# Kernel tuning notes

Measured on AMD Instinct MI355X. Metric: run time of the kernel, lower is better.

Reference implementation:

```python
import jax, jax.numpy as jnp
import numpy as np

DIM = 1024


def setup_inputs() -> dict:
    key = jax.random.key(0)
    ks = jax.random.split(key, 9)
    s = 1.0 / np.sqrt(DIM)
    x = jax.random.normal(ks[0], (4, 4096, DIM), dtype=jnp.float32)
    Wq = jax.random.uniform(ks[1], (DIM, DIM), jnp.float32, -s, s)
    bq = jax.random.uniform(ks[2], (DIM,), jnp.float32, -s, s)
    Wk = jax.random.uniform(ks[3], (DIM, DIM), jnp.float32, -s, s)
    bk = jax.random.uniform(ks[4], (DIM,), jnp.float32, -s, s)
    Wv = jax.random.uniform(ks[5], (DIM, DIM), jnp.float32, -s, s)
    bv = jax.random.uniform(ks[6], (DIM,), jnp.float32, -s, s)
    Wo = jax.random.uniform(ks[7], (DIM, DIM), jnp.float32, -s, s)
    bo = jax.random.uniform(ks[8], (DIM,), jnp.float32, -s, s)
    return {"x": x, "Wq": Wq, "bq": bq, "Wk": Wk, "bk": bk,
            "Wv": Wv, "bv": bv, "Wo": Wo, "bo": bo}


def reference(x, Wq, bq, Wk, bk, Wv, bv, Wo, bo):
    # x: [B, N, C]; weights stored as [C, C] (torch Linear applies x @ W.T,
    # here we store W already transposed so x @ W matches).
    scale = x.shape[-1] ** (-0.5)
    q = x @ Wq + bq                                  # [B, N, C]
    k = x @ Wk + bk
    v = x @ Wv + bv
    scores = jnp.einsum('bnc,bmc->bnm', q, k) * scale  # [B, N, N]
    attn = jax.nn.softmax(scores, axis=-1)
    out = jnp.einsum('bnm,bmc->bnc', attn, v)          # [B, N, C]
    return out @ Wo + bo
```

## Files before the change

kernel.cpp:

```cpp
#include <hip/hip_runtime.h>
#include <hip/hip_bf16.h>
#include <stdint.h>

typedef __bf16 bf16_8 __attribute__((ext_vector_type(8)));
typedef float  f32x4  __attribute__((ext_vector_type(4)));

#define GLL(g, l) __builtin_amdgcn_global_load_lds(                         \
    (__attribute__((address_space(1))) void*)(g),                           \
    (__attribute__((address_space(3))) void*)(l), 16, 0, 0)

__global__ void sniff_dtype(const uint32_t* __restrict__ x, uint32_t* __restrict__ flag)
{
    uint32_t w = x[threadIdx.x];
    uint32_t e = (w >> 23) & 0xFF;
    int isf32 = (e >= 100 && e <= 145) ? 1 : 0;
    unsigned long long m = __ballot(isf32);
    if (threadIdx.x == 0) *flag = (__popcll(m) >= 48) ? 1u : 0u;
}

__global__ __launch_bounds__(256)
void convert_to_bf16(const void* __restrict__ in, long elemOff,
                     __bf16* __restrict__ out, long n, const uint32_t* __restrict__ flag)
{
    long i = ((long)blockIdx.x * 256 + threadIdx.x) * 8;
    if (i >= n) return;
    bf16_8 o;
    if (*flag) {
        const float* p = (const float*)in + elemOff + i;
        float4 a = *(const float4*)p;
        float4 b = *(const float4*)(p + 4);
        o[0]=(__bf16)a.x; o[1]=(__bf16)a.y; o[2]=(__bf16)a.z; o[3]=(__bf16)a.w;
        o[4]=(__bf16)b.x; o[5]=(__bf16)b.y; o[6]=(__bf16)b.z; o[7]=(__bf16)b.w;
    } else {
        o = *(const bf16_8*)((const __bf16*)in + elemOff + i);
    }
    *(bf16_8*)(out + i) = o;
}

__global__ __launch_bounds__(256)
void convert_bias4(const void* b0, const void* b1, const void* b2, const void* b3,
                   __bf16* o0, __bf16* o1, __bf16* o2, __bf16* o3,
                   const uint32_t* __restrict__ flag)
{
    const void* in = (blockIdx.x == 0) ? b0 : (blockIdx.x == 1) ? b1
                   : (blockIdx.x == 2) ? b2 : b3;
    __bf16* out = (blockIdx.x == 0) ? o0 : (blockIdx.x == 1) ? o1
                : (blockIdx.x == 2) ? o2 : o3;
    long i = (long)threadIdx.x * 8;
    if (i >= 1024) return;
    bf16_8 o;
    if (*flag) {
        const float* p = (const float*)in + i;
        float4 a = *(const float4*)p;
        float4 b = *(const float4*)(p + 4);
        o[0]=(__bf16)a.x; o[1]=(__bf16)a.y; o[2]=(__bf16)a.z; o[3]=(__bf16)a.w;
        o[4]=(__bf16)b.x; o[5]=(__bf16)b.y; o[6]=(__bf16)b.z; o[7]=(__bf16)b.w;
    } else {
        o = *(const bf16_8*)((const __bf16*)in + i);
    }
    *(bf16_8*)(out + i) = o;
}

__global__ __launch_bounds__(256)
void convT_w4(const void* W0, const void* W1, const void* W2, const void* W3,
              __bf16* T0, __bf16* T1, __bf16* T2, __bf16* T3,
              const uint32_t* __restrict__ flag)
{
    const void* W = (blockIdx.z == 0) ? W0 : (blockIdx.z == 1) ? W1
                  : (blockIdx.z == 2) ? W2 : W3;
    __bf16* WT    = (blockIdx.z == 0) ? T0 : (blockIdx.z == 1) ? T1
                  : (blockIdx.z == 2) ? T2 : T3;
    __shared__ __bf16 tile[64][72];
    const int bc = blockIdx.x * 64, br = blockIdx.y * 64;
    const int c = threadIdx.x & 63, r0 = threadIdx.x >> 6;
    const bool f32 = (*flag != 0);
#pragma unroll
    for (int i = 0; i < 16; i++) {
        int r = i * 4 + r0;
        long idx = (long)(br + r) * 1024 + bc + c;
        float v = f32 ? ((const float*)W)[idx] : (float)((const __bf16*)W)[idx];
        tile[r][c] = (__bf16)v;
    }
    __syncthreads();
#pragma unroll
    for (int i = 0; i < 16; i++) {
        int r = i * 4 + r0;
        WT[(long)(bc + r) * 1024 + br + c] = tile[c][r];
    }
}

template<int BN_T, int OUT_MODE, bool HAS_BIAS>
__global__ __launch_bounds__(256)
void gemm_bt(const __bf16* __restrict__ A, int lda,
             const __bf16* __restrict__ BT, int ldb,
             void* __restrict__ C, int ldc,
             const __bf16* __restrict__ bias,
             int M, int N, int kLen, long zCbytes, float scale,
             float* __restrict__ rowSums)
{
    constexpr int NT    = (BN_T == 128) ? 4 : 2;
    constexpr int BHALF = BN_T * 32;
    __shared__ __align__(16) __bf16 As[2][2 * 128 * 32];
    __shared__ __align__(16) __bf16 Bs[2][2 * BHALF];

    const int t    = threadIdx.x;
    const int wave = t >> 6;
    const int lane = t & 63;
    const int quad = lane >> 4;
    const int lrow = lane & 15;
    const int wm   = wave >> 1;
    const int wn   = wave & 1;
    const long m0  = (long)blockIdx.y * 128;
    const long n0  = (long)blockIdx.x * BN_T;

    A  += (long)blockIdx.z * kLen;
    BT += (long)blockIdx.z * kLen;
    C   = (void*)((char*)C + (long)blockIdx.z * zCbytes);

    const int sr = lane >> 2;
    const int sc = (lane & 3) ^ ((lane >> 3) & 3);

    const __bf16* aSrc = A + (m0 + wave * 32 + sr) * (long)lda + sc * 8;
    const __bf16* bSrc = (BN_T == 128)
        ? BT + (n0 + wave * 32 + sr) * (long)ldb + sc * 8
        : BT + (n0 + wave * 16 + sr) * (long)ldb + sc * 8;
    const long a16 = 16L * lda, b16 = 16L * ldb;

    f32x4 zero4 = {0.f, 0.f, 0.f, 0.f};
    f32x4 acc[4][NT];
#pragma unroll
    for (int mt = 0; mt < 4; mt++)
#pragma unroll
        for (int nt = 0; nt < NT; nt++) acc[mt][nt] = zero4;

    const int sl = (lrow >> 1) & 3;

    auto STAGE = [&](int buf, const __bf16* aS, const __bf16* bS) {
        __bf16* aD = &As[buf][0] + wave * 1024;
        __bf16* bD = &Bs[buf][0] + wave * (BN_T == 128 ? 1024 : 512);
        GLL(aS, aD);
        GLL(aS + a16, aD + 512);
        GLL(bS, bD);
        if (BN_T == 128) GLL(bS + b16, bD + 512);
        GLL(aS + 32, aD + 4096);
        GLL(aS + a16 + 32, aD + 4096 + 512);
        GLL(bS + 32, bD + BHALF);
        if (BN_T == 128) GLL(bS + b16 + 32, bD + BHALF + 512);
    };

    auto COMPUTE = [&](int buf) {
#pragma unroll
        for (int kk = 0; kk < 2; kk++) {
            bf16_8 af[4], bfr[NT];
#pragma unroll
            for (int mt = 0; mt < 4; mt++)
                af[mt] = *(const bf16_8*)(&As[buf][0] + kk * 4096
                           + (wm * 64 + mt * 16 + lrow) * 32 + (quad ^ sl) * 8);
#pragma unroll
            for (int nt = 0; nt < NT; nt++)
                bfr[nt] = *(const bf16_8*)(&Bs[buf][0] + kk * BHALF
                           + (wn * (BN_T / 2) + nt * 16 + lrow) * 32 + (quad ^ sl) * 8);

#pragma unroll
            for (int mt = 0; mt < 4; mt++)
#pragma unroll
                for (int nt = 0; nt < NT; nt++)
                    acc[mt][nt] = __builtin_amdgcn_mfma_f32_16x16x32_bf16(
                                      af[mt], bfr[nt], acc[mt][nt], 0, 0, 0);
        }
    };

    STAGE(0, aSrc, bSrc);
    aSrc += 64; bSrc += 64;
    __syncthreads();

    int cur = 0;
    for (int k0 = 64; k0 < kLen; k0 += 64) {
        STAGE(cur ^ 1, aSrc, bSrc);
        aSrc += 64; bSrc += 64;
        __builtin_amdgcn_s_setprio(1);
        COMPUTE(cur);
        __builtin_amdgcn_s_setprio(0);
        __syncthreads();
        cur ^= 1;
    }
    __builtin_amdgcn_s_setprio(1);
    COMPUTE(cur);
    __builtin_amdgcn_s_setprio(0);

    if (OUT_MODE == 3) {
#pragma unroll
        for (int mt = 0; mt < 4; mt++) {
#pragma unroll
            for (int i = 0; i < 4; i++) {
                long row = m0 + wm * 64 + mt * 16 + quad * 4 + i;
                float rs = 0.f;
#pragma unroll
                for (int nt = 0; nt < NT; nt++) {
                    long col = n0 + wn * (BN_T / 2) + nt * 16 + lrow;
                    float e = exp2f(acc[mt][nt][i] * scale);
                    ((__bf16*)C)[row * (long)ldc + col] = (__bf16)e;
                    rs += e;
                }
                rs += __shfl_xor(rs, 1);
                rs += __shfl_xor(rs, 2);
                rs += __shfl_xor(rs, 4);
                rs += __shfl_xor(rs, 8);
                if (lrow == 0) atomicAdd(&rowSums[row], rs);
            }
        }
        return;
    }

#pragma unroll
    for (int mt = 0; mt < 4; mt++) {
#pragma unroll
        for (int nt = 0; nt < NT; nt++) {
#pragma unroll
            for (int i = 0; i < 4; i++) {
                long row = m0 + wm * 64 + mt * 16 + quad * 4 + i;
                long col = n0 + wn * (BN_T / 2) + nt * 16 + lrow;
                float v = acc[mt][nt][i] * scale;
                if (HAS_BIAS) v += (float)bias[col];
                if (OUT_MODE == 0)      ((__bf16*)C)[row * (long)ldc + col] = (__bf16)v;
                else if (OUT_MODE == 1) ((__bf16*)C)[col * (long)ldc + row] = (__bf16)v;
                else                    ((float* )C)[row * (long)ldc + col] = v;
            }
        }
    }
}

__global__ __launch_bounds__(256)
void softmax_f32_to_bf16(float* __restrict__ S)
{
    float* srow = S + (long)blockIdx.x * 4096;
    __bf16* prow = (__bf16*)srow;
    const int t  = threadIdx.x;
    const int wv = t >> 6, ln = t & 63;

    float4 vv[4];
    float m = -1e30f;
#pragma unroll
    for (int i = 0; i < 4; i++) {
        vv[i] = ((const float4*)srow)[t + i * 256];
        m = fmaxf(m, fmaxf(fmaxf(vv[i].x, vv[i].y), fmaxf(vv[i].z, vv[i].w)));
    }
#pragma unroll
    for (int o = 32; o; o >>= 1) m = fmaxf(m, __shfl_xor(m, o));
    __shared__ float redm[4];
    if (ln == 0) redm[wv] = m;
    __syncthreads();
    m = fmaxf(fmaxf(redm[0], redm[1]), fmaxf(redm[2], redm[3]));

    const float L2E = 1.4426950408889634f;
    float s = 0.f;
#pragma unroll
    for (int i = 0; i < 4; i++) {
        vv[i].x = exp2f((vv[i].x - m) * L2E);
        vv[i].y = exp2f((vv[i].y - m) * L2E);
        vv[i].z = exp2f((vv[i].z - m) * L2E);
        vv[i].w = exp2f((vv[i].w - m) * L2E);
        s += vv[i].x + vv[i].y + vv[i].z + vv[i].w;
    }
#pragma unroll
    for (int o = 32; o; o >>= 1) s += __shfl_xor(s, o);
    __shared__ float reds[4];
    if (ln == 0) reds[wv] = s;
    __syncthreads();
    s = reds[0] + reds[1] + reds[2] + reds[3];
    float inv = 1.f / s;

    __syncthreads();
#pragma unroll
    for (int i = 0; i < 4; i++) {
        long base = (long)(t + i * 256) * 4;
        prow[base + 0] = (__bf16)(vv[i].x * inv);
        prow[base + 1] = (__bf16)(vv[i].y * inv);
        prow[base + 2] = (__bf16)(vv[i].z * inv);
        prow[base + 3] = (__bf16)(vv[i].w * inv);
    }
}

__global__ __launch_bounds__(256)
void reduce2_to_bf16(const float* __restrict__ Sf, __bf16* __restrict__ ao)
{
    const long i = blockIdx.x;
    const float* p = Sf + 4096 * i + 2048;
    const int t = threadIdx.x;
    float4 a = ((const float4*)p)[t];
    float4 b = ((const float4*)(p + 1024))[t];
    __bf16* o = ao + i * 1024 + t * 4;
    o[0] = (__bf16)(a.x + b.x);
    o[1] = (__bf16)(a.y + b.y);
    o[2] = (__bf16)(a.z + b.z);
    o[3] = (__bf16)(a.w + b.w);
}

__global__ __launch_bounds__(256)
void reduce2_scaled(const float* __restrict__ part, const float* __restrict__ sums,
                    __bf16* __restrict__ ao)
{
    const long i = blockIdx.x;
    const float inv = 1.0f / sums[i];
    const float* p = part + i * 2048;
    const int t = threadIdx.x;
    float4 a = ((const float4*)p)[t];
    float4 b = ((const float4*)(p + 1024))[t];
    __bf16* o = ao + i * 1024 + t * 4;
    o[0] = (__bf16)((a.x + b.x) * inv);
    o[1] = (__bf16)((a.y + b.y) * inv);
    o[2] = (__bf16)((a.z + b.z) * inv);
    o[3] = (__bf16)((a.w + b.w) * inv);
}

__global__ void fill_const_f32(float* p, long n, float val)
{
    long i = (long)blockIdx.x * 256 + threadIdx.x;
    if (i < n) p[i] = val;
}

extern "C" void kernel_launch(void* const* d_in, const int* in_sizes, int n_in,
                              void* d_out, int out_size, void* d_ws, size_t ws_size,
                              hipStream_t stream)
{
    const void* x  = d_in[0];
    const void* Wq = d_in[1];
    const void* bq = d_in[2];
    const void* Wk = d_in[3];
    const void* bk = d_in[4];
    const void* Wv = d_in[5];
    const void* bv = d_in[6];
    const void* Wo = d_in[7];
    const void* bo = d_in[8];

    const int  Bb = 4, Nn = 4096, Cc = 1024;
    const long seqB = (long)Nn * Cc;
    const long allR = (long)Bb * Nn;

    auto pad = [](size_t b) { return (b + 255) & ~(size_t)255; };
    const size_t szW    = (size_t)Cc * Cc * 2;
    const size_t szBias = (size_t)Cc * 2;
    const size_t szSeq  = (size_t)seqB * 2;
    const size_t szAll  = (size_t)allR * Cc * 2;

    const size_t fixed = pad(256) + 4 * pad(szW) + 4 * pad(szBias) + pad(szAll);
    const size_t needB = fixed + 4 * pad(szSeq);
    const size_t needA = fixed + 4 * pad(szAll);

    dim3 blk(256);

    if (ws_size < needB) {
        float val = 3000.0f + (float)(ws_size >> 20);
        fill_const_f32<<<dim3((out_size + 255) / 256), blk, 0, stream>>>(
            (float*)d_out, out_size, val);
        return;
    }

    const bool batched = (ws_size >= needA);

    char* ws = (char*)d_ws;
    size_t off = 0;
    auto alloc = [&](size_t bytes) -> char* { char* p = ws + off; off += pad(bytes); return p; };

    uint32_t* flag = (uint32_t*)alloc(256);
    __bf16* WqT = (__bf16*)alloc(szW);
    __bf16* WkT = (__bf16*)alloc(szW);
    __bf16* WvT = (__bf16*)alloc(szW);
    __bf16* WoT = (__bf16*)alloc(szW);
    __bf16* bqc = (__bf16*)alloc(szBias);
    __bf16* bkc = (__bf16*)alloc(szBias);
    __bf16* bvc = (__bf16*)alloc(szBias);
    __bf16* boc = (__bf16*)alloc(szBias);
    __bf16* ao  = (__bf16*)alloc(szAll);
    const size_t tierSz = batched ? szAll : szSeq;
    __bf16* xc  = (__bf16*)alloc(tierSz);
    __bf16* q   = (__bf16*)alloc(tierSz);
    __bf16* k   = (__bf16*)alloc(tierSz);
    __bf16* vT  = (__bf16*)alloc(tierSz);

    sniff_dtype<<<dim3(1), dim3(64), 0, stream>>>((const uint32_t*)x, flag);
    convT_w4<<<dim3(16, 16, 4), blk, 0, stream>>>(Wq, Wk, Wv, Wo, WqT, WkT, WvT, WoT, flag);
    convert_bias4<<<dim3(4), blk, 0, stream>>>(bq, bk, bv, bo, bqc, bkc, bvc, boc, flag);

    const float scale    = 0.03125f;
    const float scaleL2E = 0.03125f * 1.4426950408889634f;

    if (batched) {
        convert_to_bf16<<<dim3(allR * Cc / 2048), blk, 0, stream>>>(x, 0, xc, allR * Cc, flag);
        dim3 gProj(Cc / 128, allR / 128);
        gemm_bt<128, 0, true><<<gProj, blk, 0, stream>>>(xc, Cc, WqT, Cc, q,  Cc,  bqc, (int)allR, Cc, Cc, 0, 1.f, nullptr);
        gemm_bt<128, 0, true><<<gProj, blk, 0, stream>>>(xc, Cc, WkT, Cc, k,  Cc,  bkc, (int)allR, Cc, Cc, 0, 1.f, nullptr);
        gemm_bt<128, 1, true><<<gProj, blk, 0, stream>>>(xc, Cc, WvT, Cc, vT, (int)allR, bvc, (int)allR, Cc, Cc, 0, 1.f, nullptr);

        float* sums4 = (float*)xc;
        fill_const_f32<<<dim3(64), blk, 0, stream>>>(sums4, 4L * Nn, 0.f);

        __bf16* P   = (__bf16*)d_out;
        float* part = (float*)((char*)d_out + (size_t)Nn * Nn * 2);

        for (int b = 0; b < Bb; b++) {
            const __bf16* qb  = q + (long)b * seqB;
            const __bf16* kb  = k + (long)b * seqB;
            const __bf16* vTb = vT + (long)b * Nn;
            float* sums = sums4 + (long)b * Nn;

            gemm_bt<128, 3, false><<<dim3(Nn / 128, Nn / 128), blk, 0, stream>>>(
                qb, Cc, kb, Cc, P, Nn, nullptr, Nn, Nn, Cc, 0, scaleL2E, sums);

            gemm_bt<128, 2, false><<<dim3(Cc / 128, Nn / 128, 2), blk, 0, stream>>>(
                P, Nn, vTb, (int)allR, part, 2048,
                nullptr, Nn, Cc, Nn / 2, 4096 , 1.f, nullptr);

            reduce2_scaled<<<dim3(Nn), blk, 0, stream>>>(
                part, sums, ao + (long)b * seqB);
        }
    } else {
        float* S = (float*)d_out;
        for (int b = 0; b < Bb; b++) {
            convert_to_bf16<<<dim3(seqB / 2048), blk, 0, stream>>>(x, b * seqB, xc, seqB, flag);
            dim3 gProj(Cc / 64, Nn / 128);
            gemm_bt<64, 0, true><<<gProj, blk, 0, stream>>>(xc, Cc, WqT, Cc, q,  Cc, bqc, Nn, Cc, Cc, 0, 1.f, nullptr);
            gemm_bt<64, 0, true><<<gProj, blk, 0, stream>>>(xc, Cc, WkT, Cc, k,  Cc, bkc, Nn, Cc, Cc, 0, 1.f, nullptr);
            gemm_bt<64, 1, true><<<gProj, blk, 0, stream>>>(xc, Cc, WvT, Cc, vT, Nn, bvc, Nn, Cc, Cc, 0, 1.f, nullptr);

            gemm_bt<128, 2, false><<<dim3(Nn / 128, Nn / 128), blk, 0, stream>>>(
                q, Cc, k, Cc, S, Nn, nullptr, Nn, Nn, Cc, 0, scale, nullptr);

            softmax_f32_to_bf16<<<dim3(Nn), blk, 0, stream>>>(S);

            gemm_bt<128, 2, false><<<dim3(Cc / 128, Nn / 128, 2), blk, 0, stream>>>(
                (const __bf16*)S, 2 * Nn, vT, Nn, (float*)S + 2048, Nn,
                nullptr, Nn, Cc, Nn / 2, 4096, 1.f, nullptr);

            reduce2_to_bf16<<<dim3(Nn), blk, 0, stream>>>(S, ao + (long)b * seqB);
        }
    }

    gemm_bt<128, 2, true><<<dim3(Cc / 128, (int)(allR / 128)), blk, 0, stream>>>(
        ao, Cc, WoT, Cc, (float*)d_out, Cc, boc, (int)allR, Cc, Cc, 0, 1.f, nullptr);
}
```

Before: 776.1 us.

## Add 256x256 tile 512-thread GEMM with manual waitcnt pipelining

Adds a new gemm_big kernel with 8 waves, 256x256 (or 256x128) tiles and explicit vmcnt/lgkmcnt waits plus raw barriers, so the next stage's loads stay in flight while the current stage computes. The batched path now uses it for the QKV projections, the QK^T-exp kernel, the PV kernel and the output projection. The goal is more data reuse per block and better overlap of global loads with MFMA work. In exchange, larger tiles mean fewer blocks (under one wave of blocks for some grids), higher register and LDS pressure, and hand-written wait counts that must match the number of loads in flight. It also removes setprio from the old gemm_bt, which now only runs on the fallback path.

After: 803.9 us. +3.6%, slower.

```diff
diff --git a/kernel.cpp b/kernel.cpp
--- a/kernel.cpp
+++ b/kernel.cpp
@@ -89,6 +89,158 @@
     }
 }
 
+template<int BM_T, int BN_T, int OUT_MODE, bool HAS_BIAS>
+__global__ __launch_bounds__(512, 2)
+void gemm_big(const __bf16* __restrict__ A, int lda,
+              const __bf16* __restrict__ BT, int ldb,
+              void* __restrict__ C, int ldc,
+              const __bf16* __restrict__ bias,
+              int kLen, long zCbytes, float scale,
+              float* __restrict__ rowSums)
+{
+    constexpr int MT  = BM_T / 32;
+    constexpr int NT  = BN_T / 64;
+    constexpr int AG  = BM_T / 128;
+    constexpr int BG  = BN_T / 128;
+    constexpr int NLD = 2 * (AG + BG);
+
+    __shared__ __align__(16) __bf16 As[2][2 * BM_T * 32];
+    __shared__ __align__(16) __bf16 Bs[2][2 * BN_T * 32];
+
+    const int t    = threadIdx.x;
+    const int wave = t >> 6;
+    const int lane = t & 63;
+    const int quad = lane >> 4;
+    const int lrow = lane & 15;
+    const int wm   = wave >> 2;
+    const int wn   = wave & 3;
+    const long m0  = (long)blockIdx.y * BM_T;
+    const long n0  = (long)blockIdx.x * BN_T;
+
+    A  += (long)blockIdx.z * kLen;
+    BT += (long)blockIdx.z * kLen;
+    C   = (void*)((char*)C + (long)blockIdx.z * zCbytes);
+
+    const int sr = lane >> 2;
+    const int sc = (lane & 3) ^ ((lane >> 3) & 3);
+    const int sl = (lrow >> 1) & 3;
+
+    const __bf16* aSrc = A + (m0 + wave * (BM_T / 8) + sr) * (long)lda + sc * 8;
+    const __bf16* bSrc = BT + (n0 + wave * (BN_T / 8) + sr) * (long)ldb + sc * 8;
+
+    f32x4 zero4 = {0.f, 0.f, 0.f, 0.f};
+    f32x4 acc[MT][NT];
+#pragma unroll
+    for (int mt = 0; mt < MT; mt++)
+#pragma unroll
+        for (int nt = 0; nt < NT; nt++) acc[mt][nt] = zero4;
+
+    auto STAGE = [&](int buf, const __bf16* aS, const __bf16* bS) {
+        __bf16* aD = &As[buf][0] + wave * (BM_T / 8) * 32;
+        __bf16* bD = &Bs[buf][0] + wave * (BN_T / 8) * 32;
+#pragma unroll
+        for (int kk = 0; kk < 2; kk++) {
+#pragma unroll
+            for (int g = 0; g < AG; g++)
+                GLL(aS + kk * 32 + (long)g * 16 * lda,
+                    aD + kk * (BM_T * 32) + g * 512);
+#pragma unroll
+            for (int g = 0; g < BG; g++)
+                GLL(bS + kk * 32 + (long)g * 16 * ldb,
+                    bD + kk * (BN_T * 32) + g * 512);
+        }
+    };
+
+    auto COMPUTE = [&](int buf) {
+#pragma unroll
+        for (int kk = 0; kk < 2; kk++) {
+            bf16_8 af[MT], bfr[NT];
+#pragma unroll
+            for (int mt = 0; mt < MT; mt++)
+                af[mt] = *(const bf16_8*)(&As[buf][0] + kk * (BM_T * 32)
+                           + (wm * (BM_T / 2) + mt * 16 + lrow) * 32 + (quad ^ sl) * 8);
+#pragma unroll
+            for (int nt = 0; nt < NT; nt++)
+                bfr[nt] = *(const bf16_8*)(&Bs[buf][0] + kk * (BN_T * 32)
+                           + (wn * (BN_T / 4) + nt * 16 + lrow) * 32 + (quad ^ sl) * 8);
+
+#pragma unroll
+            for (int mt = 0; mt < MT; mt++)
+#pragma unroll
+                for (int nt = 0; nt < NT; nt++)
+                    acc[mt][nt] = __builtin_amdgcn_mfma_f32_16x16x32_bf16(
+                                      af[mt], bfr[nt], acc[mt][nt], 0, 0, 0);
+        }
+    };
+
+    STAGE(0, aSrc, bSrc);
+    aSrc += 64; bSrc += 64;
+
+    int cur = 0;
+    for (int k0 = 64; k0 < kLen; k0 += 64) {
+        STAGE(cur ^ 1, aSrc, bSrc);
+        aSrc += 64; bSrc += 64;
+        if constexpr (NLD == 8) asm volatile("s_waitcnt vmcnt(8)" ::: "memory");
+        else                    asm volatile("s_waitcnt vmcnt(6)" ::: "memory");
+        __builtin_amdgcn_s_barrier();
+        __builtin_amdgcn_sched_barrier(0);
+        __builtin_amdgcn_s_setprio(1);
+        COMPUTE(cur);
+        __builtin_amdgcn_s_setprio(0);
+        asm volatile("s_waitcnt lgkmcnt(0)" ::: "memory");
+        __builtin_amdgcn_s_barrier();
+        __builtin_amdgcn_sched_barrier(0);
+        cur ^= 1;
+    }
+    asm volatile("s_waitcnt vmcnt(0)" ::: "memory");
+    __builtin_amdgcn_s_barrier();
+    __builtin_amdgcn_sched_barrier(0);
+    __builtin_amdgcn_s_setprio(1);
+    COMPUTE(cur);
+    __builtin_amdgcn_s_setprio(0);
+
+    if (OUT_MODE == 3) {
+#pragma unroll
+        for (int mt = 0; mt < MT; mt++) {
+#pragma unroll
+            for (int i = 0; i < 4; i++) {
+                long row = m0 + wm * (BM_T / 2) + mt * 16 + quad * 4 + i;
+                float rs = 0.f;
+#pragma unroll
+                for (int nt = 0; nt < NT; nt++) {
+                    long col = n0 + wn * (BN_T / 4) + nt * 16 + lrow;
+                    float e = exp2f(acc[mt][nt][i] * scale);
+                    ((__bf16*)C)[row * (long)ldc + col] = (__bf16)e;
+                    rs += e;
+                }
+                rs += __shfl_xor(rs, 1);
+                rs += __shfl_xor(rs, 2);
+                rs += __shfl_xor(rs, 4);
+                rs += __shfl_xor(rs, 8);
+                if (lrow == 0) atomicAdd(&rowSums[row], rs);
+            }
+        }
+        return;
+    }
+
+#pragma unroll
+    for (int mt = 0; mt < MT; mt++) {
+#pragma unroll
+        for (int nt = 0; nt < NT; nt++) {
+#pragma unroll
+            for (int i = 0; i < 4; i++) {
+                long row = m0 + wm * (BM_T / 2) + mt * 16 + quad * 4 + i;
+                long col = n0 + wn * (BN_T / 4) + nt * 16 + lrow;
+                float v = acc[mt][nt][i] * scale;
+                if (HAS_BIAS) v += (float)bias[col];
+                if (OUT_MODE == 0)      ((__bf16*)C)[row * (long)ldc + col] = (__bf16)v;
+                else if (OUT_MODE == 1) ((__bf16*)C)[col * (long)ldc + row] = (__bf16)v;
+                else                    ((float* )C)[row * (long)ldc + col] = v;
+            }
+        }
+    }
+}
+
 template<int BN_T, int OUT_MODE, bool HAS_BIAS>
 __global__ __launch_bounds__(256)
 void gemm_bt(const __bf16* __restrict__ A, int lda,
@@ -178,15 +330,11 @@
     for (int k0 = 64; k0 < kLen; k0 += 64) {
         STAGE(cur ^ 1, aSrc, bSrc);
         aSrc += 64; bSrc += 64;
-        __builtin_amdgcn_s_setprio(1);
         COMPUTE(cur);
-        __builtin_amdgcn_s_setprio(0);
         __syncthreads();
         cur ^= 1;
     }
-    __builtin_amdgcn_s_setprio(1);
     COMPUTE(cur);
-    __builtin_amdgcn_s_setprio(0);
 
     if (OUT_MODE == 3) {
 #pragma unroll
@@ -348,6 +496,7 @@
     const size_t needA = fixed + 4 * pad(szAll);
 
     dim3 blk(256);
+    dim3 blk5(512);
 
     if (ws_size < needB) {
         float val = 3000.0f + (float)(ws_size >> 20);
@@ -387,10 +536,10 @@
 
     if (batched) {
         convert_to_bf16<<<dim3(allR * Cc / 2048), blk, 0, stream>>>(x, 0, xc, allR * Cc, flag);
-        dim3 gProj(Cc / 128, allR / 128);
-        gemm_bt<128, 0, true><<<gProj, blk, 0, stream>>>(xc, Cc, WqT, Cc, q,  Cc,  bqc, (int)allR, Cc, Cc, 0, 1.f, nullptr);
-        gemm_bt<128, 0, true><<<gProj, blk, 0, stream>>>(xc, Cc, WkT, Cc, k,  Cc,  bkc, (int)allR, Cc, Cc, 0, 1.f, nullptr);
-        gemm_bt<128, 1, true><<<gProj, blk, 0, stream>>>(xc, Cc, WvT, Cc, vT, (int)allR, bvc, (int)allR, Cc, Cc, 0, 1.f, nullptr);
+        dim3 gProj(Cc / 256, allR / 256);
+        gemm_big<256, 256, 0, true><<<gProj, blk5, 0, stream>>>(xc, Cc, WqT, Cc, q,  Cc,  bqc, Cc, 0, 1.f, nullptr);
+        gemm_big<256, 256, 0, true><<<gProj, blk5, 0, stream>>>(xc, Cc, WkT, Cc, k,  Cc,  bkc, Cc, 0, 1.f, nullptr);
+        gemm_big<256, 256, 1, true><<<gProj, blk5, 0, stream>>>(xc, Cc, WvT, Cc, vT, (int)allR, bvc, Cc, 0, 1.f, nullptr);
 
         float* sums4 = (float*)xc;
         fill_const_f32<<<dim3(64), blk, 0, stream>>>(sums4, 4L * Nn, 0.f);
@@ -404,16 +553,19 @@
             const __bf16* vTb = vT + (long)b * Nn;
             float* sums = sums4 + (long)b * Nn;
 
-            gemm_bt<128, 3, false><<<dim3(Nn / 128, Nn / 128), blk, 0, stream>>>(
-                qb, Cc, kb, Cc, P, Nn, nullptr, Nn, Nn, Cc, 0, scaleL2E, sums);
-
-            gemm_bt<128, 2, false><<<dim3(Cc / 128, Nn / 128, 2), blk, 0, stream>>>(
+            gemm_big<256, 256, 3, false><<<dim3(Nn / 256, Nn / 256), blk5, 0, stream>>>(
+                qb, Cc, kb, Cc, P, Nn, nullptr, Cc, 0, scaleL2E, sums);
+
+            gemm_big<256, 128, 2, false><<<dim3(Cc / 128, Nn / 256, 2), blk5, 0, stream>>>(
                 P, Nn, vTb, (int)allR, part, 2048,
-                nullptr, Nn, Cc, Nn / 2, 4096 , 1.f, nullptr);
+                nullptr, Nn / 2, 4096 , 1.f, nullptr);
 
             reduce2_scaled<<<dim3(Nn), blk, 0, stream>>>(
                 part, sums, ao + (long)b * seqB);
         }
+
+        gemm_big<256, 256, 2, true><<<dim3(Cc / 256, (int)(allR / 256)), blk5, 0, stream>>>(
+            ao, Cc, WoT, Cc, (float*)d_out, Cc, boc, Cc, 0, 1.f, nullptr);
     } else {
         float* S = (float*)d_out;
         for (int b = 0; b < Bb; b++) {
@@ -434,8 +586,8 @@
 
             reduce2_to_bf16<<<dim3(Nn), blk, 0, stream>>>(S, ao + (long)b * seqB);
         }
-    }
-
-    gemm_bt<128, 2, true><<<dim3(Cc / 128, (int)(allR / 128)), blk, 0, stream>>>(
-        ao, Cc, WoT, Cc, (float*)d_out, Cc, boc, (int)allR, Cc, Cc, 0, 1.f, nullptr);
-}
+
+        gemm_bt<128, 2, true><<<dim3(Cc / 128, (int)(allR / 128)), blk, 0, stream>>>(
+            ao, Cc, WoT, Cc, (float*)d_out, Cc, boc, (int)allR, Cc, Cc, 0, 1.f, nullptr);
+    }
+}
```
